# Optimization experiments

Measured on AMD Instinct MI355X. Metric: run time of the kernel, lower is better.

The kernel has to match this reference:

```python
import jax, jax.numpy as jnp
import numpy as np

BS, L, S, AMB = 64, 64, 63, 32   # batch, sentence len, opseq steps, ambiguities per step
H, E, V, MLP = 128, 300, 50000, 1024
EPS = 1e-8


def setup_inputs() -> dict:
    key = jax.random.key(0)
    ks = jax.random.split(key, 12)
    u = lambda k, shp: jax.random.uniform(k, shp, dtype=jnp.float32) * 0.1
    return {
        "sentences1": jax.random.randint(ks[0], (BS, L), 0, V, dtype=jnp.int32),
        "operations1": jax.random.randint(ks[1], (BS, S, 2 * AMB), 0, L, dtype=jnp.int32),
        "oopl1": jnp.full((BS,), L + S, dtype=jnp.int32),
        "sentences2": jax.random.randint(ks[2], (BS, L), 0, V, dtype=jnp.int32),
        "operations2": jax.random.randint(ks[3], (BS, S, 2 * AMB), 0, L, dtype=jnp.int32),
        "oopl2": jnp.full((BS,), L + S, dtype=jnp.int32),
        "W": u(ks[4], (5 * H, E)),
        "U": u(ks[5], (5 * H, 2 * H)),
        "b": jnp.zeros((5 * H,), dtype=jnp.float32),
        "energy_u": u(ks[6], (H,)),
        "unk_embedding": u(ks[7], (E,)),
        "word_embeddings": jax.random.normal(ks[8], (V, E), dtype=jnp.float32),
        "A": u(ks[9], (MLP, 4 * H)),
        "a": u(ks[10], (MLP,)),
        "inv_temperature": jnp.float32(1.0),
    }


def _gates(preact, ccL, ccR):
    # preact: [..., 5H]; tree-LSTM cell (i, fL, fR, o, u gates)
    i = jax.nn.sigmoid(preact[..., :H])
    fL = jax.nn.sigmoid(preact[..., H:2 * H])
    fR = jax.nn.sigmoid(preact[..., 2 * H:3 * H])
    o = jax.nn.sigmoid(preact[..., 3 * H:4 * H])
    u = jnp.tanh(preact[..., 4 * H:5 * H])
    c = fL * ccL + fR * ccR + i * u
    h = o * jnp.tanh(c)
    return c, h


def _run_chart(sentences, operations, W, U, b, energy_u, unk_embedding,
               word_embeddings, inv_temperature):
    bs = sentences.shape[0]
    # leaf phase: embed each word, preact = W @ emb + b, ccL = ccR = 0
    emb = jnp.where(sentences[..., None] >= 0,
                    word_embeddings[jnp.clip(sentences, 0)], unk_embedding)  # [bs,L,E]
    preact = jnp.einsum('ble,ge->blg', emb, W) + b                            # [bs,L,5H]
    c, h = _gates(preact, 0.0, 0.0)
    chart = jnp.zeros((bs, L + S, 2 * H), dtype=jnp.float32)
    chart = chart.at[:, :L, :].set(jnp.concatenate([c, h], axis=-1))

    def step(chart, inp):
        ops, pos = inp                                   # ops: [bs, 2*AMB], pos: scalar
        entries = jnp.take_along_axis(chart, ops[:, :, None].astype(jnp.int32), axis=1)
        entries = entries.reshape(bs, AMB, 2, 2 * H)     # [bs, amb, (L,R), 2H]
        ccL = entries[:, :, 0, :H]
        ccR = entries[:, :, 1, :H]
        hh = entries[:, :, :, H:].reshape(bs, AMB, 2 * H)  # concat(hL, hR)
        pre = jnp.einsum('bak,gk->bag', hh, U) + b         # [bs, amb, 5H]
        c, h = _gates(pre, ccL, ccR)
        # cosine similarity of h against energy_u
        hn = jnp.maximum(jnp.sqrt(jnp.sum(h * h, axis=-1)), EPS)
        un = jnp.maximum(jnp.sqrt(jnp.sum(energy_u * energy_u)), EPS)
        e = jnp.einsum('bah,h->ba', h, energy_u) / (hn * un)
        s = jax.nn.softmax(e * inv_temperature, axis=1)    # [bs, amb]
        combined = jnp.concatenate([jnp.einsum('ba,bah->bh', s, c),
                                    jnp.einsum('ba,bah->bh', s, h)], axis=-1)
        chart = jax.lax.dynamic_update_slice(chart, combined[:, None, :], (0, pos, 0))
        return chart, None

    ops_seq = jnp.swapaxes(operations, 0, 1)             # [S, bs, 2*AMB]
    positions = L + jnp.arange(S, dtype=jnp.int32)
    chart, _ = jax.lax.scan(step, chart, (ops_seq, positions))
    return chart


def reference(sentences1, operations1, oopl1, sentences2, operations2, oopl2,
              W, U, b, energy_u, unk_embedding, word_embeddings, A, a,
              inv_temperature):
    chart1 = _run_chart(sentences1, operations1, W, U, b, energy_u,
                        unk_embedding, word_embeddings, inv_temperature)
    chart2 = _run_chart(sentences2, operations2, W, U, b, energy_u,
                        unk_embedding, word_embeddings, inv_temperature)
    bs = chart1.shape[0]
    bidx = jnp.arange(bs)
    s1 = chart1[bidx, oopl1 - 1, H:]                     # final composed h, [bs, H]
    s2 = chart2[bidx, oopl2 - 1, H:]
    u = (s1 - s2) ** 2
    v = s1 * s2
    conc = jnp.concatenate([u, v, s1, s2], axis=1)       # [bs, 4H]
    out = jax.nn.relu(jnp.einsum('jk,ik->ij', A, conc) + a)
    return out
```

## Files before the change

kernel.cpp:

```cpp
#include <hip/hip_runtime.h>
#include <hip/hip_bf16.h>

#define BSZ 64
#define LL  64
#define SS  63
#define AMB 32
#define HH  128
#define EE  300
#define MLPN 1024
#define GG  640
#define K2  256
#define PP  127
#define CROW 272

typedef __attribute__((ext_vector_type(8))) short short8;
typedef __attribute__((ext_vector_type(4))) float f32x4;

__device__ __forceinline__ float sigf(float x) { return 1.f / (1.f + __expf(-x)); }

__device__ __forceinline__ unsigned short f2bf(float x) {
    unsigned int u = __float_as_uint(x);
    u += 0x7fffu + ((u >> 16) & 1u);
    return (unsigned short)(u >> 16);
}
__device__ __forceinline__ float bf2f(short x) {
    return __uint_as_float(((unsigned)(unsigned short)x) << 16);
}

#define PW 25600
#define PU 20480
__global__ void __launch_bounds__(256) prep_kernel(
        const float* __restrict__ W, const float* __restrict__ U,
        short* __restrict__ WTB, short* __restrict__ UTB) {
    int idx = blockIdx.x * 256 + threadIdx.x;
    if (idx < PW) {
        int lane = idx & 63, r = idx >> 6;
        int kk = r % 10, n = r / 10;
        int g = n * 16 + (lane & 15);
        int k0 = kk * 32 + ((lane >> 4) << 3);
        const float* src = W + (size_t)g * EE + k0;
        float f[8];
        if (k0 + 8 <= EE) {
            f32x4 x0 = *(const f32x4*)src;
            f32x4 x1 = *(const f32x4*)(src + 4);
            f[0]=x0[0]; f[1]=x0[1]; f[2]=x0[2]; f[3]=x0[3];
            f[4]=x1[0]; f[5]=x1[1]; f[6]=x1[2]; f[7]=x1[3];
        } else {
#pragma unroll
            for (int j = 0; j < 8; ++j) f[j] = (k0 + j < EE) ? src[j] : 0.f;
        }
        short8 v;
#pragma unroll
        for (int j = 0; j < 8; ++j) v[j] = (short)f2bf(f[j]);
        *(short8*)(WTB + (size_t)idx * 8) = v;
    } else if (idx < PW + PU) {
        int o = idx - PW;
        int lane = o & 63, r = o >> 6;
        int kk = r & 7, n = r >> 3;
        int g = n * 16 + (lane & 15);
        int k0 = kk * 32 + ((lane >> 4) << 3);
        const float* src = U + (size_t)g * K2 + k0;
        f32x4 x0 = *(const f32x4*)src;
        f32x4 x1 = *(const f32x4*)(src + 4);
        short8 v;
        v[0]=(short)f2bf(x0[0]); v[1]=(short)f2bf(x0[1]); v[2]=(short)f2bf(x0[2]); v[3]=(short)f2bf(x0[3]);
        v[4]=(short)f2bf(x1[0]); v[5]=(short)f2bf(x1[1]); v[6]=(short)f2bf(x1[2]); v[7]=(short)f2bf(x1[3]);
        *(short8*)(UTB + (size_t)o * 8) = v;
    }
}

__global__ void __launch_bounds__(1024, 4) main_kernel(
        const int* __restrict__ sent1, const int* __restrict__ sent2,
        const int* __restrict__ ops1, const int* __restrict__ ops2,
        const int* __restrict__ oopl1, const int* __restrict__ oopl2,
        const short* __restrict__ WTB, const short* __restrict__ UTB,
        const float* __restrict__ bias, const float* __restrict__ eu,
        const float* __restrict__ invt,
        const float* __restrict__ unk, const float* __restrict__ wemb,
        float* __restrict__ fin) {
    __shared__ __align__(16) short chartL[127 * CROW + 16];
    __shared__ __align__(16) char  buf[40960];
    __shared__ int ops_all[SS * 64];
    __shared__ int sent_lds[64];
    __shared__ unsigned long long smask[64];
    __shared__ int live_list[SS];
    __shared__ float e_num[AMB], h2s[AMB], s_w[AMB];
    __shared__ float comb[2][2][HH];
    __shared__ int nl_sh;
    __shared__ float un_sh;

    short8* AsL = (short8*)buf;
    short8* As2 = (short8*)buf;
    float*  chh = (float*)(buf + 16384);

    const int tid = threadIdx.x;
    const int pair = blockIdx.x, ch = pair >> 6, b = pair & 63;
    const int* sent = ch ? sent2 : sent1;
    const int* ops  = ch ? ops2 : ops1;
    const int* oopl = ch ? oopl2 : oopl1;
    const float it = invt[0];
    const int w = tid >> 6, lane = tid & 63, quad = lane >> 4, l15 = lane & 15;

#pragma unroll
    for (int i = 0; i < 4; ++i) {
        int idx = i * 1024 + tid;
        if (idx < SS * 64) ops_all[idx] = min(max(ops[b * SS * 64 + idx], 0), PP - 1);
    }
    if (tid < 64) sent_lds[tid] = sent[b * LL + tid];
    if (tid < 64) {
        float v = eu[tid] * eu[tid] + eu[tid + 64] * eu[tid + 64];
        for (int off = 32; off >= 1; off >>= 1) v += __shfl_xor(v, off);
        if (tid == 0) un_sh = fmaxf(sqrtf(v), 1e-8f);
    }
    __syncthreads();

#pragma unroll
    for (int i = 0; i < 4; ++i) {
        int t = i * 16 + w;
        if (t < SS) {
            int q = ops_all[t * 64 + lane] - LL;
            unsigned long long bit = (q >= 0 && q < t) ? (1ull << q) : 0ull;
            for (int off = 32; off >= 1; off >>= 1) bit |= __shfl_xor(bit, off);
            if (lane == 0) smask[t] = bit;
        }
    }
    __syncthreads();

    if (tid == 0) {
        unsigned long long mask = 0ull;
        int q0 = oopl[b] - 1 - LL;
        if (q0 >= 0) { if (q0 > SS - 1) q0 = SS - 1; mask = 1ull << q0; }
        for (int t = SS - 1; t >= 1; --t)
            if ((mask >> t) & 1) mask |= smask[t];
        int n = 0;
        for (int t = 0; t < SS; ++t)
            if ((mask >> t) & 1) live_list[n++] = t;
        nl_sh = n;
    }

#pragma unroll
    for (int i = 0; i < 3; ++i) {
        int idx = i * 1024 + tid;
        if (idx < 2142)
            ((int4*)(chartL + 64 * CROW))[idx] = make_int4(0, 0, 0, 0);
    }
    for (int i = 0; i < 3; ++i) {
        int slot = i * 1024 + tid;
        if (slot < 2560) {
            int t = slot / 40, oct = slot - t * 40;
            int s = sent_lds[t];
            const float* src = (s >= 0) ? (wemb + (size_t)s * EE) : unk;
            int k0 = oct * 8;
            short8 v;
            if (k0 + 8 <= EE) {
                f32x4 x0 = *(const f32x4*)(src + k0);
                f32x4 x1 = *(const f32x4*)(src + k0 + 4);
                v[0]=(short)f2bf(x0[0]); v[1]=(short)f2bf(x0[1]);
                v[2]=(short)f2bf(x0[2]); v[3]=(short)f2bf(x0[3]);
                v[4]=(short)f2bf(x1[0]); v[5]=(short)f2bf(x1[1]);
                v[6]=(short)f2bf(x1[2]); v[7]=(short)f2bf(x1[3]);
            } else {
#pragma unroll
                for (int j = 0; j < 8; ++j)
                    v[j] = (short)f2bf((k0 + j < EE) ? src[k0 + j] : 0.f);
            }
            AsL[((t >> 4) * 10 + (oct >> 2)) * 64 + ((oct & 3) << 4) + (t & 15)] = v;
        }
    }
    __syncthreads();

    {
        const int mt = w & 3, nug = w >> 2;
        f32x4 acc[2][3] = {};
        for (int kk = 0; kk < 10; ++kk) {
            short8 a0 = AsL[(mt * 10 + kk) * 64 + lane];
#pragma unroll
            for (int si = 0; si < 3; ++si) {
                int s5 = (si == 0) ? 0 : (si == 1 ? 3 : 4);
#pragma unroll
                for (int hf = 0; hf < 2; ++hf) {
                    int n = (nug + hf * 4) + 8 * s5;
                    short8 bv = *(const short8*)(WTB + ((size_t)(n * 10 + kk) * 64 + lane) * 8);
                    acc[hf][si] = __builtin_amdgcn_mfma_f32_16x16x32_bf16(a0, bv, acc[hf][si], 0, 0, 0);
                }
            }
        }
#pragma unroll
        for (int hf = 0; hf < 2; ++hf) {
            int jc = (nug + hf * 4) * 16 + l15;
            float bi = bias[jc], bo = bias[3 * HH + jc], bu = bias[4 * HH + jc];
#pragma unroll
            for (int r = 0; r < 4; ++r) {
                float pi = acc[hf][0][r] + bi;
                float po = acc[hf][1][r] + bo;
                float pu = acc[hf][2][r] + bu;
                float cv = sigf(pi) * tanhf(pu);
                float hv = sigf(po) * tanhf(cv);
                int l = mt * 16 + quad * 4 + r;
                chartL[l * CROW + jc]      = (short)f2bf(cv);
                chartL[l * CROW + HH + jc] = (short)f2bf(hv);
            }
        }
    }
    __syncthreads();

    const int nl = nl_sh;
    const float eul = eu[lane], euh = eu[64 + lane];
    const int smt = w & 1, snu = w >> 1;
    const int sjc = snu * 16 + l15;
    const float bi  = bias[sjc],          bfl = bias[HH + sjc];
    const float bfr = bias[2 * HH + sjc], bo  = bias[3 * HH + sjc];
    const float bu  = bias[4 * HH + sjc];

    for (int sidx = 0; sidx < nl; ++sidx) {
        const int t = live_list[sidx];
        const int* oprow = ops_all + t * 64;

        {
            int a = tid >> 5, oct = tid & 31, side = oct >> 4, m8 = oct & 15;
            int row = oprow[2 * a + side];
            short8 v = *(const short8*)(chartL + row * CROW + HH + m8 * 8);
            As2[((a >> 4) * 8 + (oct >> 2)) * 64 + ((oct & 3) << 4) + (a & 15)] = v;
        }
        __syncthreads();

        float cvals[4], hvals[4];
        {
            f32x4 acc[5] = {};
            for (int kk = 0; kk < 8; ++kk) {
                short8 a0 = As2[(smt * 8 + kk) * 64 + lane];
#pragma unroll
                for (int s5 = 0; s5 < 5; ++s5) {
                    short8 bv = *(const short8*)(UTB + ((size_t)((snu + 8 * s5) * 8 + kk) * 64 + lane) * 8);
                    acc[s5] = __builtin_amdgcn_mfma_f32_16x16x32_bf16(a0, bv, acc[s5], 0, 0, 0);
                }
            }
#pragma unroll
            for (int r = 0; r < 4; ++r) {
                int a = smt * 16 + quad * 4 + r;
                float ccLv = bf2f(chartL[oprow[2 * a] * CROW + sjc]);
                float ccRv = bf2f(chartL[oprow[2 * a + 1] * CROW + sjc]);
                float cv = sigf(acc[1][r] + bfl) * ccLv
                         + sigf(acc[2][r] + bfr) * ccRv
                         + sigf(acc[0][r] + bi) * tanhf(acc[4][r] + bu);
                float hv = sigf(acc[3][r] + bo) * tanhf(cv);
                cvals[r] = cv; hvals[r] = hv;
                chh[a * 132 + sjc] = hv;
            }
        }
        __syncthreads();

#pragma unroll
        for (int i = 0; i < 2; ++i) {
            int a = w * 2 + i;
            float h0 = chh[a * 132 + lane], h1 = chh[a * 132 + 64 + lane];
            float pe = h0 * eul + h1 * euh;
            float pn = h0 * h0 + h1 * h1;
            for (int off = 32; off >= 1; off >>= 1) {
                pe += __shfl_xor(pe, off);
                pn += __shfl_xor(pn, off);
            }
            if (lane == 0) { e_num[a] = pe; h2s[a] = pn; }
        }
        __syncthreads();

        if (tid < 64) {
            float v = (tid < AMB)
                ? (e_num[tid] / (fmaxf(sqrtf(h2s[tid]), 1e-8f) * un_sh)) * it
                : -3.4e38f;
            float m = v;
            for (int off = 32; off >= 1; off >>= 1) m = fmaxf(m, __shfl_xor(m, off));
            float ex = (tid < AMB) ? __expf(v - m) : 0.f;
            float su = ex;
            for (int off = 32; off >= 1; off >>= 1) su += __shfl_xor(su, off);
            if (tid < AMB) s_w[tid] = ex / su;
        }
        __syncthreads();

        {
            float sc = 0.f, sh = 0.f;
#pragma unroll
            for (int r = 0; r < 4; ++r) {
                int a = smt * 16 + quad * 4 + r;
                float sw = s_w[a];
                sc = fmaf(sw, cvals[r], sc);
                sh = fmaf(sw, hvals[r], sh);
            }
            sc += __shfl_xor(sc, 16); sc += __shfl_xor(sc, 32);
            sh += __shfl_xor(sh, 16); sh += __shfl_xor(sh, 32);
            if (lane < 16) {
                comb[smt][0][sjc] = sc;
                comb[smt][1][sjc] = sh;
            }
        }
        __syncthreads();
        if (tid < K2) {
            int part = tid >> 7, col = tid & 127;
            float val = comb[0][part][col] + comb[1][part][col];
            chartL[(LL + t) * CROW + part * HH + col] = (short)f2bf(val);
        }
        __syncthreads();
    }

    int p = min(max(oopl[b] - 1, 0), PP - 1);
    if (tid < K2)
        fin[(size_t)pair * K2 + tid] = bf2f(chartL[p * CROW + tid]);
}

__global__ void __launch_bounds__(256) mlp_kernel(
        const float* __restrict__ fin,
        const float* __restrict__ A, const float* __restrict__ abias,
        float* __restrict__ out) {
    __shared__ __align__(16) float conc[4][512];
    const int tid = threadIdx.x;
    const int jt = blockIdx.x & 15, bt = blockIdx.x >> 4;

#pragma unroll
    for (int i = 0; i < 2; ++i) {
        int s = i * 256 + tid;
        int bl = s >> 7, kv = s & 127;
        int k0 = kv * 4, sel = k0 >> 7, kk0 = k0 & 127;
        int b = bt * 4 + bl;
        f32x4 s1 = *(const f32x4*)(fin + (size_t)b * K2 + HH + kk0);
        f32x4 s2 = *(const f32x4*)(fin + (size_t)(BSZ + b) * K2 + HH + kk0);
        f32x4 v;
        if (sel == 0)      { f32x4 d = s1 - s2; v = d * d; }
        else if (sel == 1) v = s1 * s2;
        else if (sel == 2) v = s1;
        else               v = s2;
        *(f32x4*)&conc[bl][k0] = v;
    }
    __syncthreads();

    const int jj = tid & 63, bg = tid >> 6;
    const int j = jt * 64 + jj, b = bt * 4 + bg;
    const float* Arow = A + (size_t)j * 512;
    float acc0 = abias[j], acc1 = 0.f;
    for (int k = 0; k < 512; k += 8) {
        f32x4 a0 = *(const f32x4*)(Arow + k);
        f32x4 a1 = *(const f32x4*)(Arow + k + 4);
        f32x4 c0 = *(const f32x4*)&conc[bg][k];
        f32x4 c1 = *(const f32x4*)&conc[bg][k + 4];
#pragma unroll
        for (int u = 0; u < 4; ++u) {
            acc0 = fmaf(a0[u], c0[u], acc0);
            acc1 = fmaf(a1[u], c1[u], acc1);
        }
    }
    out[(size_t)b * MLPN + j] = fmaxf(acc0 + acc1, 0.f);
}

extern "C" void kernel_launch(void* const* d_in, const int* in_sizes, int n_in,
                              void* d_out, int out_size, void* d_ws, size_t ws_size,
                              hipStream_t stream) {
    const int*   sent1 = (const int*)d_in[0];
    const int*   ops1  = (const int*)d_in[1];
    const int*   oopl1 = (const int*)d_in[2];
    const int*   sent2 = (const int*)d_in[3];
    const int*   ops2  = (const int*)d_in[4];
    const int*   oopl2 = (const int*)d_in[5];
    const float* W     = (const float*)d_in[6];
    const float* U     = (const float*)d_in[7];
    const float* bias  = (const float*)d_in[8];
    const float* eu    = (const float*)d_in[9];
    const float* unk   = (const float*)d_in[10];
    const float* wemb  = (const float*)d_in[11];
    const float* A     = (const float*)d_in[12];
    const float* ab    = (const float*)d_in[13];
    const float* invt  = (const float*)d_in[14];
    float* out = (float*)d_out;
    (void)in_sizes; (void)n_in; (void)out_size; (void)ws_size;

    char* ws = (char*)d_ws;
    const size_t WTB_OFF = 0;
    const size_t UTB_OFF = 409600;
    const size_t FIN_OFF = 737280;
    short* WTB = (short*)(ws + WTB_OFF);
    short* UTB = (short*)(ws + UTB_OFF);
    float* fin = (float*)(ws + FIN_OFF);

    prep_kernel<<<180, 256, 0, stream>>>(W, U, WTB, UTB);

    main_kernel<<<128, 1024, 0, stream>>>(sent1, sent2, ops1, ops2, oopl1, oopl2,
                                          WTB, UTB, bias, eu, invt, unk, wemb, fin);

    mlp_kernel<<<256, 256, 0, stream>>>(fin, A, ab, out);
}
```

Measured before the change: 188.6 us.

## Halve main kernel block to 512 threads with two column tiles per wave

The main chart kernel drops from 1024 to 512 threads per block, and each wave now handles two column tiles in the leaf and composition GEMMs, carrying register arrays for both. Bias is staged once in LDS, and the serial single-thread live-step list construction becomes a wave-parallel shuffle plus popcount scan. The goal is cheaper barriers and less serial setup on the latency-bound recurrent loop. The cost is more work per wave, so each step's GEMM and gate math runs longer.

```diff
diff --git a/kernel.cpp b/kernel.cpp
--- a/kernel.cpp
+++ b/kernel.cpp
@@ -69,7 +69,7 @@
     }
 }
 
-__global__ void __launch_bounds__(1024, 4) main_kernel(
+__global__ void __launch_bounds__(512, 2) main_kernel(
         const int* __restrict__ sent1, const int* __restrict__ sent2,
         const int* __restrict__ ops1, const int* __restrict__ ops2,
         const int* __restrict__ oopl1, const int* __restrict__ oopl2,
@@ -81,6 +81,7 @@
     __shared__ __align__(16) short chartL[127 * CROW + 16];
     __shared__ __align__(16) char  buf[40960];
     __shared__ int ops_all[SS * 64];
+    __shared__ float bias_lds[GG];
     __shared__ int sent_lds[64];
     __shared__ unsigned long long smask[64];
     __shared__ int live_list[SS];
@@ -102,9 +103,14 @@
     const int w = tid >> 6, lane = tid & 63, quad = lane >> 4, l15 = lane & 15;
 
 #pragma unroll
-    for (int i = 0; i < 4; ++i) {
-        int idx = i * 1024 + tid;
+    for (int i = 0; i < 8; ++i) {
+        int idx = i * 512 + tid;
         if (idx < SS * 64) ops_all[idx] = min(max(ops[b * SS * 64 + idx], 0), PP - 1);
+    }
+#pragma unroll
+    for (int i = 0; i < 2; ++i) {
+        int idx = i * 512 + tid;
+        if (idx < GG) bias_lds[idx] = bias[idx];
     }
     if (tid < 64) sent_lds[tid] = sent[b * LL + tid];
     if (tid < 64) {
@@ -115,8 +121,8 @@
     __syncthreads();
 
 #pragma unroll
-    for (int i = 0; i < 4; ++i) {
-        int t = i * 16 + w;
+    for (int i = 0; i < 8; ++i) {
+        int t = i * 8 + w;
         if (t < SS) {
             int q = ops_all[t * 64 + lane] - LL;
             unsigned long long bit = (q >= 0 && q < t) ? (1ull << q) : 0ull;
@@ -126,51 +132,50 @@
     }
     __syncthreads();
 
-    if (tid == 0) {
+    if (tid < 64) {
+        unsigned long long mym = (lane < SS) ? smask[lane] : 0ull;
         unsigned long long mask = 0ull;
         int q0 = oopl[b] - 1 - LL;
         if (q0 >= 0) { if (q0 > SS - 1) q0 = SS - 1; mask = 1ull << q0; }
         for (int t = SS - 1; t >= 1; --t)
-            if ((mask >> t) & 1) mask |= smask[t];
-        int n = 0;
-        for (int t = 0; t < SS; ++t)
-            if ((mask >> t) & 1) live_list[n++] = t;
-        nl_sh = n;
-    }
-
-#pragma unroll
-    for (int i = 0; i < 3; ++i) {
-        int idx = i * 1024 + tid;
+            if ((mask >> t) & 1) mask |= __shfl(mym, t);
+        if (lane < SS && ((mask >> lane) & 1))
+            live_list[__popcll(mask & ((1ull << lane) - 1ull))] = lane;
+        if (lane == 0) nl_sh = (int)__popcll(mask);
+    }
+
+#pragma unroll
+    for (int i = 0; i < 5; ++i) {
+        int idx = i * 512 + tid;
         if (idx < 2142)
             ((int4*)(chartL + 64 * CROW))[idx] = make_int4(0, 0, 0, 0);
     }
-    for (int i = 0; i < 3; ++i) {
-        int slot = i * 1024 + tid;
-        if (slot < 2560) {
-            int t = slot / 40, oct = slot - t * 40;
-            int s = sent_lds[t];
-            const float* src = (s >= 0) ? (wemb + (size_t)s * EE) : unk;
-            int k0 = oct * 8;
-            short8 v;
-            if (k0 + 8 <= EE) {
-                f32x4 x0 = *(const f32x4*)(src + k0);
-                f32x4 x1 = *(const f32x4*)(src + k0 + 4);
-                v[0]=(short)f2bf(x0[0]); v[1]=(short)f2bf(x0[1]);
-                v[2]=(short)f2bf(x0[2]); v[3]=(short)f2bf(x0[3]);
-                v[4]=(short)f2bf(x1[0]); v[5]=(short)f2bf(x1[1]);
-                v[6]=(short)f2bf(x1[2]); v[7]=(short)f2bf(x1[3]);
-            } else {
-#pragma unroll
-                for (int j = 0; j < 8; ++j)
-                    v[j] = (short)f2bf((k0 + j < EE) ? src[k0 + j] : 0.f);
-            }
-            AsL[((t >> 4) * 10 + (oct >> 2)) * 64 + ((oct & 3) << 4) + (t & 15)] = v;
-        }
-    }
-    __syncthreads();
-
-    {
-        const int mt = w & 3, nug = w >> 2;
+    for (int i = 0; i < 5; ++i) {
+        int slot = i * 512 + tid;
+        int t = slot / 40, oct = slot - t * 40;
+        int s = sent_lds[t];
+        const float* src = (s >= 0) ? (wemb + (size_t)s * EE) : unk;
+        int k0 = oct * 8;
+        short8 v;
+        if (k0 + 8 <= EE) {
+            f32x4 x0 = *(const f32x4*)(src + k0);
+            f32x4 x1 = *(const f32x4*)(src + k0 + 4);
+            v[0]=(short)f2bf(x0[0]); v[1]=(short)f2bf(x0[1]);
+            v[2]=(short)f2bf(x0[2]); v[3]=(short)f2bf(x0[3]);
+            v[4]=(short)f2bf(x1[0]); v[5]=(short)f2bf(x1[1]);
+            v[6]=(short)f2bf(x1[2]); v[7]=(short)f2bf(x1[3]);
+        } else {
+#pragma unroll
+            for (int j = 0; j < 8; ++j)
+                v[j] = (short)f2bf((k0 + j < EE) ? src[k0 + j] : 0.f);
+        }
+        AsL[((t >> 4) * 10 + (oct >> 2)) * 64 + ((oct & 3) << 4) + (t & 15)] = v;
+    }
+    __syncthreads();
+
+    for (int cc = 0; cc < 2; ++cc) {
+        const int tk = cc * 8 + w;
+        const int mt = tk & 3, nug = tk >> 2;
         f32x4 acc[2][3] = {};
         for (int kk = 0; kk < 10; ++kk) {
             short8 a0 = AsL[(mt * 10 + kk) * 64 + lane];
@@ -188,7 +193,7 @@
 #pragma unroll
         for (int hf = 0; hf < 2; ++hf) {
             int jc = (nug + hf * 4) * 16 + l15;
-            float bi = bias[jc], bo = bias[3 * HH + jc], bu = bias[4 * HH + jc];
+            float bi = bias_lds[jc], bo = bias_lds[3 * HH + jc], bu = bias_lds[4 * HH + jc];
 #pragma unroll
             for (int r = 0; r < 4; ++r) {
                 float pi = acc[hf][0][r] + bi;
@@ -206,26 +211,27 @@
 
     const int nl = nl_sh;
     const float eul = eu[lane], euh = eu[64 + lane];
-    const int smt = w & 1, snu = w >> 1;
-    const int sjc = snu * 16 + l15;
-    const float bi  = bias[sjc],          bfl = bias[HH + sjc];
-    const float bfr = bias[2 * HH + sjc], bo  = bias[3 * HH + sjc];
-    const float bu  = bias[4 * HH + sjc];
+    const int smt = w & 1, snu0 = w >> 1;
 
     for (int sidx = 0; sidx < nl; ++sidx) {
         const int t = live_list[sidx];
         const int* oprow = ops_all + t * 64;
 
-        {
-            int a = tid >> 5, oct = tid & 31, side = oct >> 4, m8 = oct & 15;
+#pragma unroll
+        for (int i = 0; i < 2; ++i) {
+            int slot = i * 512 + tid;
+            int a = slot >> 5, oct = slot & 31, side = oct >> 4, m8 = oct & 15;
             int row = oprow[2 * a + side];
             short8 v = *(const short8*)(chartL + row * CROW + HH + m8 * 8);
             As2[((a >> 4) * 8 + (oct >> 2)) * 64 + ((oct & 3) << 4) + (a & 15)] = v;
         }
         __syncthreads();
 
-        float cvals[4], hvals[4];
-        {
+        float cvals[2][4], hvals[2][4];
+#pragma unroll
+        for (int cc = 0; cc < 2; ++cc) {
+            const int snu = snu0 + cc * 4;
+            const int sjc = snu * 16 + l15;
             f32x4 acc[5] = {};
             for (int kk = 0; kk < 8; ++kk) {
                 short8 a0 = As2[(smt * 8 + kk) * 64 + lane];
@@ -235,6 +241,9 @@
                     acc[s5] = __builtin_amdgcn_mfma_f32_16x16x32_bf16(a0, bv, acc[s5], 0, 0, 0);
                 }
             }
+            float bi  = bias_lds[sjc],          bfl = bias_lds[HH + sjc];
+            float bfr = bias_lds[2 * HH + sjc], bo  = bias_lds[3 * HH + sjc];
+            float bu  = bias_lds[4 * HH + sjc];
 #pragma unroll
             for (int r = 0; r < 4; ++r) {
                 int a = smt * 16 + quad * 4 + r;
@@ -244,15 +253,15 @@
                          + sigf(acc[2][r] + bfr) * ccRv
                          + sigf(acc[0][r] + bi) * tanhf(acc[4][r] + bu);
                 float hv = sigf(acc[3][r] + bo) * tanhf(cv);
-                cvals[r] = cv; hvals[r] = hv;
+                cvals[cc][r] = cv; hvals[cc][r] = hv;
                 chh[a * 132 + sjc] = hv;
             }
         }
         __syncthreads();
 
 #pragma unroll
-        for (int i = 0; i < 2; ++i) {
-            int a = w * 2 + i;
+        for (int i = 0; i < 4; ++i) {
+            int a = w * 4 + i;
             float h0 = chh[a * 132 + lane], h1 = chh[a * 132 + 64 + lane];
             float pe = h0 * eul + h1 * euh;
             float pn = h0 * h0 + h1 * h1;
@@ -277,14 +286,16 @@
         }
         __syncthreads();
 
-        {
+#pragma unroll
+        for (int cc = 0; cc < 2; ++cc) {
+            const int sjc = (snu0 + cc * 4) * 16 + l15;
             float sc = 0.f, sh = 0.f;
 #pragma unroll
             for (int r = 0; r < 4; ++r) {
                 int a = smt * 16 + quad * 4 + r;
                 float sw = s_w[a];
-                sc = fmaf(sw, cvals[r], sc);
-                sh = fmaf(sw, hvals[r], sh);
+                sc = fmaf(sw, cvals[cc][r], sc);
+                sh = fmaf(sw, hvals[cc][r], sh);
             }
             sc += __shfl_xor(sc, 16); sc += __shfl_xor(sc, 32);
             sh += __shfl_xor(sh, 16); sh += __shfl_xor(sh, 32);
@@ -381,8 +392,8 @@
 
     prep_kernel<<<180, 256, 0, stream>>>(W, U, WTB, UTB);
 
-    main_kernel<<<128, 1024, 0, stream>>>(sent1, sent2, ops1, ops2, oopl1, oopl2,
-                                          WTB, UTB, bias, eu, invt, unk, wemb, fin);
+    main_kernel<<<128, 512, 0, stream>>>(sent1, sent2, ops1, ops2, oopl1, oopl2,
+                                         WTB, UTB, bias, eu, invt, unk, wemb, fin);
 
     mlp_kernel<<<256, 256, 0, stream>>>(fin, A, ab, out);
 }
```

New measurement: 202.5 us. +7.4%, slower.
